# Kernel tuning notes

Hardware: AMD Instinct MI355X
Metric: run time of the kernel (lower is better)

Reference implementation:

```python
import jax, jax.numpy as jnp
import numpy as np

NUM_CLASSES = 5
B, D, H, W = 4, 64, 256, 256


def _per_class_counts(labels, weights, num_classes):
    # labels: [B, N] int, weights: [B, N] float -> [B, C] float counts
    b = labels.shape[0]
    ids = labels + jnp.arange(b, dtype=labels.dtype)[:, None] * num_classes
    counts = jax.ops.segment_sum(weights.ravel(), ids.ravel().astype(jnp.int32),
                                 num_segments=b * num_classes)
    return counts.reshape(b, num_classes)


def _dice(predicted, target, num_classes):
    b = predicted.shape[0]
    p = predicted.reshape(b, -1)  # [B, N] integer class labels
    t = target.reshape(b, -1)
    ones = jnp.ones(p.shape, dtype=jnp.float32)
    pred_sum = _per_class_counts(p, ones, num_classes)                      # sum of one-hot(pred) over voxels
    tar_sum = _per_class_counts(t, ones, num_classes)                       # sum of one-hot(target) over voxels
    inter = _per_class_counts(p, (p == t).astype(jnp.float32), num_classes) # per-class intersection counts
    num = 2.0 * inter
    den = pred_sum + tar_sum
    zero = den == 0
    num = jnp.where(zero, 1.0, num)
    den = jnp.where(zero, 1.0, den)
    return (num / den).mean(axis=0)  # [C]


def setup_inputs() -> dict:
    key = jax.random.key(0)
    k1, k2 = jax.random.split(key)
    predicted = jax.random.randint(k1, (B, D, H, W), 0, NUM_CLASSES, dtype=jnp.int32)
    target = jax.random.randint(k2, (B, D, H, W), 0, NUM_CLASSES, dtype=jnp.int32)
    return {"predicted": predicted, "target": target}


def reference(predicted, target):
    return _dice(predicted, target, NUM_CLASSES)
```

## Files before the change

kernel.cpp:

```cpp
#include <hip/hip_runtime.h>

#define NUM_CLASSES 5
#define BATCH 4
#define NPB (64 * 256 * 256)
#define VEC_PER_BATCH (NPB / 4)
#define THREADS 256
#define VECS 16
#define CHUNKV 4
#define BLOCKS_X (VEC_PER_BATCH / (THREADS * VECS))
#define SLOTS 15
#define PSTRIDE 16


__global__ __launch_bounds__(THREADS, 4) void dice_count_kernel(
    const int* __restrict__ pred, const int* __restrict__ targ,
    unsigned int* __restrict__ partial) {
  const int b = blockIdx.y;
  const int4* __restrict__ p4 = (const int4*)(pred + (long long)b * NPB);
  const int4* __restrict__ t4 = (const int4*)(targ + (long long)b * NPB);

  const int base = blockIdx.x * (THREADS * VECS) + threadIdx.x;

  unsigned accP0 = 0, accP1 = 0, accT0 = 0, accT1 = 0, accI0 = 0, accI1 = 0;

  int4 pa0, pa1, pa2, pa3, ta0, ta1, ta2, ta3;
  int4 pb0, pb1, pb2, pb3, tb0, tb1, tb2, tb3;

#define IDX(KK, CC) (base + ((KK) * CHUNKV + (CC)) * THREADS)
#define LOAD_A(KK)                                                   \
  pa0 = p4[IDX(KK, 0)]; pa1 = p4[IDX(KK, 1)];                        \
  pa2 = p4[IDX(KK, 2)]; pa3 = p4[IDX(KK, 3)];                        \
  ta0 = t4[IDX(KK, 0)]; ta1 = t4[IDX(KK, 1)];                        \
  ta2 = t4[IDX(KK, 2)]; ta3 = t4[IDX(KK, 3)];
#define LOAD_B(KK)                                                   \
  pb0 = p4[IDX(KK, 0)]; pb1 = p4[IDX(KK, 1)];                        \
  pb2 = p4[IDX(KK, 2)]; pb3 = p4[IDX(KK, 3)];                        \
  tb0 = t4[IDX(KK, 0)]; tb1 = t4[IDX(KK, 1)];                        \
  tb2 = t4[IDX(KK, 2)]; tb3 = t4[IDX(KK, 3)];

#define ACC_ELEM(PE, TE, AP, AT, AI)                   \
    {                                                  \
      const unsigned op = 1u << (6u * (unsigned)(PE)); \
      AP += op;                                        \
      AT += 1u << (6u * (unsigned)(TE));               \
      AI += ((PE) == (TE)) ? op : 0u;                  \
    }
#define CONS1(PV, TV, AP, AT, AI)                      \
    ACC_ELEM(PV.x, TV.x, AP, AT, AI)                   \
    ACC_ELEM(PV.y, TV.y, AP, AT, AI)                   \
    ACC_ELEM(PV.z, TV.z, AP, AT, AI)                   \
    ACC_ELEM(PV.w, TV.w, AP, AT, AI)
#define CONSUME_A(AP, AT, AI)                          \
    CONS1(pa0, ta0, AP, AT, AI) CONS1(pa1, ta1, AP, AT, AI) \
    CONS1(pa2, ta2, AP, AT, AI) CONS1(pa3, ta3, AP, AT, AI)
#define CONSUME_B(AP, AT, AI)                          \
    CONS1(pb0, tb0, AP, AT, AI) CONS1(pb1, tb1, AP, AT, AI) \
    CONS1(pb2, tb2, AP, AT, AI) CONS1(pb3, tb3, AP, AT, AI)

  LOAD_A(0)
  LOAD_B(1)
  __builtin_amdgcn_sched_barrier(0);
  CONSUME_A(accP0, accT0, accI0)
  LOAD_A(2)
  __builtin_amdgcn_sched_barrier(0);
  CONSUME_B(accP0, accT0, accI0)
  LOAD_B(3)
  __builtin_amdgcn_sched_barrier(0);
  CONSUME_A(accP1, accT1, accI1)
  CONSUME_B(accP1, accT1, accI1)

#define UNPACK(A0, A1, R01, R23, R4)                                     \
  unsigned R01 = ((A0 & 63u) + (A1 & 63u)) |                             \
                 ((((A0 >> 6) & 63u) + ((A1 >> 6) & 63u)) << 16);        \
  unsigned R23 = (((A0 >> 12) & 63u) + ((A1 >> 12) & 63u)) |             \
                 ((((A0 >> 18) & 63u) + ((A1 >> 18) & 63u)) << 16);      \
  unsigned R4 = ((A0 >> 24) & 63u) + ((A1 >> 24) & 63u);
  UNPACK(accP0, accP1, p01, p23, p4r)
  UNPACK(accT0, accT1, t01, t23, t4r)
  UNPACK(accI0, accI1, i01, i23, i4r)

#pragma unroll
  for (int off = 32; off >= 1; off >>= 1) {
    p01 += (unsigned)__shfl_xor((int)p01, off);
    p23 += (unsigned)__shfl_xor((int)p23, off);
    p4r += (unsigned)__shfl_xor((int)p4r, off);
    t01 += (unsigned)__shfl_xor((int)t01, off);
    t23 += (unsigned)__shfl_xor((int)t23, off);
    t4r += (unsigned)__shfl_xor((int)t4r, off);
    i01 += (unsigned)__shfl_xor((int)i01, off);
    i23 += (unsigned)__shfl_xor((int)i23, off);
    i4r += (unsigned)__shfl_xor((int)i4r, off);
  }

  __shared__ unsigned int s[SLOTS];
  if (threadIdx.x < SLOTS) s[threadIdx.x] = 0;
  __syncthreads();

  if ((threadIdx.x & 63) == 0) {
    atomicAdd(&s[0], p01 & 0xFFFFu);
    atomicAdd(&s[1], p01 >> 16);
    atomicAdd(&s[2], p23 & 0xFFFFu);
    atomicAdd(&s[3], p23 >> 16);
    atomicAdd(&s[4], p4r);
    atomicAdd(&s[5], t01 & 0xFFFFu);
    atomicAdd(&s[6], t01 >> 16);
    atomicAdd(&s[7], t23 & 0xFFFFu);
    atomicAdd(&s[8], t23 >> 16);
    atomicAdd(&s[9], t4r);
    atomicAdd(&s[10], i01 & 0xFFFFu);
    atomicAdd(&s[11], i01 >> 16);
    atomicAdd(&s[12], i23 & 0xFFFFu);
    atomicAdd(&s[13], i23 >> 16);
    atomicAdd(&s[14], i4r);
  }
  __syncthreads();

  if (threadIdx.x < SLOTS)
    partial[(b * BLOCKS_X + blockIdx.x) * PSTRIDE + threadIdx.x] = s[threadIdx.x];
}

__global__ __launch_bounds__(256) void dice_final_kernel(
    const unsigned int* __restrict__ partial, float* __restrict__ out) {
  __shared__ unsigned int red[BATCH * SLOTS][4];
  const int t = threadIdx.x;
  if (t < BATCH * SLOTS * 4) {
    const int q = t & 3;
    const int s = (t >> 2) % SLOTS;
    const int bb = (t >> 2) / SLOTS;
    unsigned int sum = 0;
    for (int j = q * (BLOCKS_X / 4); j < (q + 1) * (BLOCKS_X / 4); ++j)
      sum += partial[(bb * BLOCKS_X + j) * PSTRIDE + s];
    red[(t >> 2)][q] = sum;
  }
  __syncthreads();
  if (t < NUM_CLASSES) {
    float acc = 0.0f;
#pragma unroll
    for (int bb = 0; bb < BATCH; ++bb) {
      const int ip = bb * SLOTS + t;
      const int it = bb * SLOTS + 5 + t;
      const int ii = bb * SLOTS + 10 + t;
      const float ps = (float)(red[ip][0] + red[ip][1] + red[ip][2] + red[ip][3]);
      const float ts = (float)(red[it][0] + red[it][1] + red[it][2] + red[it][3]);
      const float is = (float)(red[ii][0] + red[ii][1] + red[ii][2] + red[ii][3]);
      float num = 2.0f * is;
      float den = ps + ts;
      if (den == 0.0f) { num = 1.0f; den = 1.0f; }
      acc += num / den;
    }
    out[t] = acc * (1.0f / BATCH);
  }
}

extern "C" void kernel_launch(void* const* d_in, const int* in_sizes, int n_in,
                              void* d_out, int out_size, void* d_ws, size_t ws_size,
                              hipStream_t stream) {
  const int* pred = (const int*)d_in[0];
  const int* targ = (const int*)d_in[1];
  float* out = (float*)d_out;
  unsigned int* partial = (unsigned int*)d_ws;

  dim3 grid(BLOCKS_X, BATCH);
  dice_count_kernel<<<grid, THREADS, 0, stream>>>(pred, targ, partial);
  dice_final_kernel<<<1, 256, 0, stream>>>(partial, out);
}
```

Measured before the change: 147.4 us.

## Replace chunked loads with inline-asm rolling load pipeline and fine-grained vmcnt waits

Replaces the A/B double-buffered chunk loads with raw global_load_dwordx4 inline asm that keeps 8 vector pairs in flight. Each consume step waits on its own load via an explicit s_waitcnt vmcnt(N), and the next pair is issued right after. The goal is to keep memory-level parallelism high and start computing as soon as each load lands, instead of waiting on whole chunks. The risk is correctness: the hand-written vmcnt counts and asm constraints must match the compiler's real instruction order, and the asm hides the loads from the compiler's scheduling.

```diff
diff --git a/kernel.cpp b/kernel.cpp
--- a/kernel.cpp
+++ b/kernel.cpp
@@ -6,37 +6,35 @@
 #define VEC_PER_BATCH (NPB / 4)
 #define THREADS 256
 #define VECS 16
-#define CHUNKV 4
 #define BLOCKS_X (VEC_PER_BATCH / (THREADS * VECS))
 #define SLOTS 15
 #define PSTRIDE 16
 
 
+typedef int v4i __attribute__((ext_vector_type(4)));
+
+#define GLOAD(Q, VOFF, SBASE) \
+  asm volatile("global_load_dwordx4 %0, %1, %2" : "=v"(Q) : "v"(VOFF), "s"(SBASE))
+
+#define WAITP(N, P, T) \
+  asm volatile("s_waitcnt vmcnt(" #N ")" : "+v"(P), "+v"(T))
+
 __global__ __launch_bounds__(THREADS, 4) void dice_count_kernel(
     const int* __restrict__ pred, const int* __restrict__ targ,
     unsigned int* __restrict__ partial) {
   const int b = blockIdx.y;
-  const int4* __restrict__ p4 = (const int4*)(pred + (long long)b * NPB);
-  const int4* __restrict__ t4 = (const int4*)(targ + (long long)b * NPB);
+  const unsigned long long pB = (unsigned long long)(
+      pred + (long long)b * NPB + (long long)blockIdx.x * (THREADS * VECS * 4));
+  const unsigned long long tB = (unsigned long long)(
+      targ + (long long)b * NPB + (long long)blockIdx.x * (THREADS * VECS * 4));
 
-  const int base = blockIdx.x * (THREADS * VECS) + threadIdx.x;
+  unsigned vo[VECS];
+#pragma unroll
+  for (int k = 0; k < VECS; ++k) vo[k] = threadIdx.x * 16u + (unsigned)k * 4096u;
+
+  v4i qp[VECS], qt[VECS];
 
   unsigned accP0 = 0, accP1 = 0, accT0 = 0, accT1 = 0, accI0 = 0, accI1 = 0;
-
-  int4 pa0, pa1, pa2, pa3, ta0, ta1, ta2, ta3;
-  int4 pb0, pb1, pb2, pb3, tb0, tb1, tb2, tb3;
-
-#define IDX(KK, CC) (base + ((KK) * CHUNKV + (CC)) * THREADS)
-#define LOAD_A(KK)                                                   \
-  pa0 = p4[IDX(KK, 0)]; pa1 = p4[IDX(KK, 1)];                        \
-  pa2 = p4[IDX(KK, 2)]; pa3 = p4[IDX(KK, 3)];                        \
-  ta0 = t4[IDX(KK, 0)]; ta1 = t4[IDX(KK, 1)];                        \
-  ta2 = t4[IDX(KK, 2)]; ta3 = t4[IDX(KK, 3)];
-#define LOAD_B(KK)                                                   \
-  pb0 = p4[IDX(KK, 0)]; pb1 = p4[IDX(KK, 1)];                        \
-  pb2 = p4[IDX(KK, 2)]; pb3 = p4[IDX(KK, 3)];                        \
-  tb0 = t4[IDX(KK, 0)]; tb1 = t4[IDX(KK, 1)];                        \
-  tb2 = t4[IDX(KK, 2)]; tb3 = t4[IDX(KK, 3)];
 
 #define ACC_ELEM(PE, TE, AP, AT, AI)                   \
     {                                                  \
@@ -46,28 +44,34 @@
       AI += ((PE) == (TE)) ? op : 0u;                  \
     }
 #define CONS1(PV, TV, AP, AT, AI)                      \
-    ACC_ELEM(PV.x, TV.x, AP, AT, AI)                   \
-    ACC_ELEM(PV.y, TV.y, AP, AT, AI)                   \
-    ACC_ELEM(PV.z, TV.z, AP, AT, AI)                   \
-    ACC_ELEM(PV.w, TV.w, AP, AT, AI)
-#define CONSUME_A(AP, AT, AI)                          \
-    CONS1(pa0, ta0, AP, AT, AI) CONS1(pa1, ta1, AP, AT, AI) \
-    CONS1(pa2, ta2, AP, AT, AI) CONS1(pa3, ta3, AP, AT, AI)
-#define CONSUME_B(AP, AT, AI)                          \
-    CONS1(pb0, tb0, AP, AT, AI) CONS1(pb1, tb1, AP, AT, AI) \
-    CONS1(pb2, tb2, AP, AT, AI) CONS1(pb3, tb3, AP, AT, AI)
+    ACC_ELEM(PV[0], TV[0], AP, AT, AI)                 \
+    ACC_ELEM(PV[1], TV[1], AP, AT, AI)                 \
+    ACC_ELEM(PV[2], TV[2], AP, AT, AI)                 \
+    ACC_ELEM(PV[3], TV[3], AP, AT, AI)
 
-  LOAD_A(0)
-  LOAD_B(1)
-  __builtin_amdgcn_sched_barrier(0);
-  CONSUME_A(accP0, accT0, accI0)
-  LOAD_A(2)
-  __builtin_amdgcn_sched_barrier(0);
-  CONSUME_B(accP0, accT0, accI0)
-  LOAD_B(3)
-  __builtin_amdgcn_sched_barrier(0);
-  CONSUME_A(accP1, accT1, accI1)
-  CONSUME_B(accP1, accT1, accI1)
+#define ISSUE(K)  GLOAD(qp[K], vo[K], pB); GLOAD(qt[K], vo[K], tB)
+#define STEP(K, N, AP, AT, AI) \
+    WAITP(N, qp[K], qt[K]);    \
+    CONS1(qp[K], qt[K], AP, AT, AI)
+
+  ISSUE(0); ISSUE(1); ISSUE(2); ISSUE(3);
+  ISSUE(4); ISSUE(5); ISSUE(6); ISSUE(7);
+  STEP(0, 14, accP0, accT0, accI0); ISSUE(8);
+  STEP(1, 14, accP0, accT0, accI0); ISSUE(9);
+  STEP(2, 14, accP0, accT0, accI0); ISSUE(10);
+  STEP(3, 14, accP0, accT0, accI0); ISSUE(11);
+  STEP(4, 14, accP0, accT0, accI0); ISSUE(12);
+  STEP(5, 14, accP0, accT0, accI0); ISSUE(13);
+  STEP(6, 14, accP0, accT0, accI0); ISSUE(14);
+  STEP(7, 14, accP0, accT0, accI0); ISSUE(15);
+  STEP(8,  14, accP1, accT1, accI1);
+  STEP(9,  12, accP1, accT1, accI1);
+  STEP(10, 10, accP1, accT1, accI1);
+  STEP(11,  8, accP1, accT1, accI1);
+  STEP(12,  6, accP1, accT1, accI1);
+  STEP(13,  4, accP1, accT1, accI1);
+  STEP(14,  2, accP1, accT1, accI1);
+  STEP(15,  0, accP1, accT1, accI1);
 
 #define UNPACK(A0, A1, R01, R23, R4)                                     \
   unsigned R01 = ((A0 & 63u) + (A1 & 63u)) |                             \
```

After: 150.4 us. +2.1%, slower.
